# Kernel tuning notes

Measured on AMD Instinct MI355X. Metric: run time of the kernel, lower is better.

Reference implementation:

```python
import jax, jax.numpy as jnp
import numpy as np

K = 9
SIGMA = 4.0
RADIUS = 16  # round(4*sigma)
IMAGE_SHAPE = (256, 256)


def _gaussian_kernel_1d():
    i = jnp.arange(2 * RADIUS + 1, dtype=jnp.float32) - RADIUS
    g = jnp.exp(-(i ** 2) / (2.0 * SIGMA ** 2))
    return g / jnp.sum(g)


def _gaussian_blur(x):
    # x: [b, H, W, 1]; separable Gaussian blur, reflect-101 borders (cv2 default)
    g = _gaussian_kernel_1d()
    xp = jnp.pad(x, ((0, 0), (RADIUS, RADIUS), (RADIUS, RADIUS), (0, 0)), mode='reflect')
    dn = ('NHWC', 'HWIO', 'NHWC')
    kv = g.reshape(2 * RADIUS + 1, 1, 1, 1)  # vertical pass
    kh = g.reshape(1, 2 * RADIUS + 1, 1, 1)  # horizontal pass
    y = jax.lax.conv_general_dilated(xp, kv, (1, 1), 'VALID', dimension_numbers=dn)
    y = jax.lax.conv_general_dilated(y, kh, (1, 1), 'VALID', dimension_numbers=dn)
    return y


def setup_inputs() -> dict:
    key = jax.random.key(0)
    k1, k2 = jax.random.split(key)
    inputs = jax.random.normal(k1, (8, 32, 32, 512), dtype=jnp.float32)
    feature_vector = jax.random.normal(k2, (16384, 512), dtype=jnp.float32)
    return {"inputs": inputs, "feature_vector": feature_vector}


def reference(inputs, feature_vector):
    b, h, w, c = inputs.shape
    feat = inputs.reshape(b * h * w, c)
    # pairwise euclidean distances: [b*h*w, N]
    d2 = (jnp.sum(feat ** 2, axis=-1, keepdims=True)
          + jnp.sum(feature_vector ** 2, axis=-1)[None, :]
          - 2.0 * feat @ feature_vector.T)
    dist = jnp.sqrt(jnp.maximum(d2, 0.0))
    # k smallest distances, ascending (equivalent to tf.sort(...)[..., :k])
    neg_topk, _ = jax.lax.top_k(-dist, K)
    score = -neg_topk  # [b*h*w, K], ascending
    mask = score[:, 0].reshape(b, h, w, 1)
    score = score.reshape(b, h * w, K)
    # patch with maximal nearest-neighbor distance
    idx = jnp.argmax(score[..., 0], axis=-1)  # [b]
    conf = jnp.take_along_axis(score, idx[:, None, None], axis=1)[:, 0, :]  # [b, K]
    exp_conf = jnp.exp(conf)
    weight = 1.0 - jnp.max(exp_conf, axis=-1) / jnp.sum(exp_conf, axis=-1)
    score_out = (jnp.max(score[..., 0], axis=-1) * weight)[:, None]  # [b, 1]
    mask = jax.image.resize(mask, (b, *IMAGE_SHAPE, 1), method='bilinear', antialias=False)
    mask = _gaussian_blur(mask)
    return score_out, mask
```

## Files before the change

### kernel.cpp

```cpp
#include <hip/hip_runtime.h>

typedef __attribute__((ext_vector_type(8))) short bf16x8;
typedef __attribute__((ext_vector_type(4))) float f32x4;

static constexpr int M = 8192;
static constexpr int N = 16384;
static constexpr int K = 512;
static constexpr int BM = 256;
static constexpr int BN = 256;
static constexpr int BK = 64;
static constexpr int KCHUNKS = K / BK;
static constexpr int RBLK = M / BM;
static constexpr int CBLK = N / BN;
static constexpr int BMs = 128;
static constexpr int BKs = 64;
static constexpr int NGROUPS_S = 8;
static constexpr int GROUP_N_S = N / NGROUPS_S;
static constexpr int NTILES_S = GROUP_N_S / 128;
static constexpr float F_INF = 3.0e38f;

__device__ __forceinline__ unsigned short f2bf(float f) {
    unsigned int u = __float_as_uint(f);
    return (unsigned short)((u + 0x7fffu + ((u >> 16) & 1u)) >> 16);
}

__device__ __forceinline__ void gl_lds16(const unsigned short* g, unsigned short* l) {
    __builtin_amdgcn_global_load_lds(
        (const __attribute__((address_space(1))) unsigned int*)g,
        (__attribute__((address_space(3))) unsigned int*)l, 16, 0, 0);
}

__global__ void k_prep(const float* __restrict__ Q, const float* __restrict__ F,
                       unsigned short* __restrict__ Qb, unsigned short* __restrict__ Fb,
                       float* __restrict__ qn, float* __restrict__ fn) {
    int wid = blockIdx.x * 4 + (threadIdx.x >> 6);
    int lane = threadIdx.x & 63;
    bool isQ = wid < M;
    const float* src = isQ ? (Q + (size_t)wid * K) : (F + (size_t)(wid - M) * K);
    unsigned short* dst = isQ ? (Qb + (size_t)wid * K) : (Fb + (size_t)(wid - M) * K);
    const float4* p = reinterpret_cast<const float4*>(src) + lane * 2;
    float4 a = p[0], b = p[1];
    float s = a.x*a.x + a.y*a.y + a.z*a.z + a.w*a.w
            + b.x*b.x + b.y*b.y + b.z*b.z + b.w*b.w;
    bf16x8 v;
    v[0]=(short)f2bf(a.x); v[1]=(short)f2bf(a.y); v[2]=(short)f2bf(a.z); v[3]=(short)f2bf(a.w);
    v[4]=(short)f2bf(b.x); v[5]=(short)f2bf(b.y); v[6]=(short)f2bf(b.z); v[7]=(short)f2bf(b.w);
    *reinterpret_cast<bf16x8*>(dst + lane * 8) = v;
    #pragma unroll
    for (int d = 1; d < 64; d <<= 1) s += __shfl_xor(s, d);
    if (lane == 0) { if (isQ) qn[wid] = s; else fn[wid - M] = s; }
}

__global__ void k_norms(const float* __restrict__ Q, const float* __restrict__ F,
                        float* __restrict__ qn, float* __restrict__ fn) {
    int wid = blockIdx.x * 4 + (threadIdx.x >> 6);
    int lane = threadIdx.x & 63;
    const float* src = (wid < M) ? (Q + (size_t)wid * K) : (F + (size_t)(wid - M) * K);
    const float4* p = reinterpret_cast<const float4*>(src) + lane * 2;
    float4 a = p[0], b = p[1];
    float s = a.x*a.x + a.y*a.y + a.z*a.z + a.w*a.w
            + b.x*b.x + b.y*b.y + b.z*b.z + b.w*b.w;
    #pragma unroll
    for (int d = 1; d < 64; d <<= 1) s += __shfl_xor(s, d);
    if (lane == 0) { if (wid < M) qn[wid] = s; else fn[wid - M] = s; }
}

__global__ __launch_bounds__(512, 2)
void k_mingemm3(const unsigned short* __restrict__ Qb, const unsigned short* __restrict__ Fb,
                const float* __restrict__ qn, const float* __restrict__ fn,
                float* __restrict__ pv, unsigned int* __restrict__ pi) {
    __shared__ unsigned short As[2][BM * BK];
    __shared__ unsigned short Bs[2][BN * BK];
    __shared__ float redv[BM][4];
    __shared__ unsigned int redi[BM][4];

    const int tid = threadIdx.x;
    const int lane = tid & 63;
    const int wave = tid >> 6;
    const int wr = wave >> 2;
    const int wc = wave & 3;
    const int l15 = lane & 15, l4 = lane >> 4;

    const int wg = blockIdx.x;
    const int x = wg & 7, q = wg >> 3;
    const int c_blk = x * 8 + (q & 7);
    const int r_blk = q >> 3;
    const int row0 = r_blk * BM;
    const int col0 = c_blk * BN;

    const int r_l = lane >> 3, p8 = lane & 7;
    const int g8 = p8 ^ r_l;
    const unsigned short* gA[4];
    const unsigned short* gB[4];
    #pragma unroll
    for (int i = 0; i < 4; ++i) {
        int row = wave * 32 + i * 8 + r_l;
        gA[i] = Qb + (size_t)(row0 + row) * K + g8 * 8;
        gB[i] = Fb + (size_t)(col0 + row) * K + g8 * 8;
    }

    auto stage = [&](int kc, int buf) {
        #pragma unroll
        for (int i = 0; i < 4; ++i) gl_lds16(gA[i] + kc * BK, &As[buf][(wave*32 + i*8) * BK]);
        #pragma unroll
        for (int i = 0; i < 4; ++i) gl_lds16(gB[i] + kc * BK, &Bs[buf][(wave*32 + i*8) * BK]);
    };

    f32x4 acc[8][4];
    #pragma unroll
    for (int a = 0; a < 8; ++a)
        #pragma unroll
        for (int b = 0; b < 4; ++b) acc[a][b] = f32x4{0.f, 0.f, 0.f, 0.f};

    stage(0, 0);
    stage(1, 1);
    asm volatile("s_waitcnt vmcnt(8)" ::: "memory");
    __builtin_amdgcn_sched_barrier(0);
    __builtin_amdgcn_s_barrier();

    for (int kc = 0; kc < KCHUNKS; ++kc) {
        const int p = kc & 1;
        bf16x8 af[4][2], bfv[4][2];
        #pragma unroll
        for (int ks = 0; ks < 2; ++ks) {
            const int gidx = ks * 4 + l4;
            #pragma unroll
            for (int fi = 0; fi < 4; ++fi) {
                int r = wr*128 + fi*16 + l15;
                int pg = gidx ^ (r & 7);
                af[fi][ks] = *reinterpret_cast<const bf16x8*>(&As[p][r*BK + pg*8]);
            }
            #pragma unroll
            for (int fj = 0; fj < 4; ++fj) {
                int r = wc*64 + fj*16 + l15;
                int pg = gidx ^ (r & 7);
                bfv[fj][ks] = *reinterpret_cast<const bf16x8*>(&Bs[p][r*BK + pg*8]);
            }
        }
        __builtin_amdgcn_s_setprio(1);
        #pragma unroll
        for (int ks = 0; ks < 2; ++ks)
            #pragma unroll
            for (int fi = 0; fi < 4; ++fi)
                #pragma unroll
                for (int fj = 0; fj < 4; ++fj)
                    acc[fi][fj] = __builtin_amdgcn_mfma_f32_16x16x32_bf16(
                        af[fi][ks], bfv[fj][ks], acc[fi][fj], 0, 0, 0);
        __builtin_amdgcn_s_setprio(0);
        bf16x8 ah[4][2];
        #pragma unroll
        for (int ks = 0; ks < 2; ++ks) {
            const int gidx = ks * 4 + l4;
            #pragma unroll
            for (int fi = 0; fi < 4; ++fi) {
                int r = wr*128 + 64 + fi*16 + l15;
                int pg = gidx ^ (r & 7);
                ah[fi][ks] = *reinterpret_cast<const bf16x8*>(&As[p][r*BK + pg*8]);
            }
        }
        asm volatile("s_waitcnt lgkmcnt(0)" ::: "memory");
        __builtin_amdgcn_sched_barrier(0);
        __builtin_amdgcn_s_barrier();
        if (kc + 2 < KCHUNKS) {
            stage(kc + 2, p);
            asm volatile("s_waitcnt vmcnt(8)" ::: "memory");
        } else {
            asm volatile("s_waitcnt vmcnt(0)" ::: "memory");
        }
        __builtin_amdgcn_sched_barrier(0);
        __builtin_amdgcn_s_barrier();
        __builtin_amdgcn_s_setprio(1);
        #pragma unroll
        for (int ks = 0; ks < 2; ++ks)
            #pragma unroll
            for (int fi = 0; fi < 4; ++fi)
                #pragma unroll
                for (int fj = 0; fj < 4; ++fj)
                    acc[4+fi][fj] = __builtin_amdgcn_mfma_f32_16x16x32_bf16(
                        ah[fi][ks], bfv[fj][ks], acc[4+fi][fj], 0, 0, 0);
        __builtin_amdgcn_s_setprio(0);
    }

    float fnv[4];
    #pragma unroll
    for (int fj = 0; fj < 4; ++fj) fnv[fj] = fn[col0 + wc*64 + fj*16 + l15];
    #pragma unroll
    for (int fi = 0; fi < 8; ++fi) {
        #pragma unroll
        for (int j = 0; j < 4; ++j) {
            int rloc = wr*128 + fi*16 + l4*4 + j;
            float qv = qn[row0 + rloc];
            float v = F_INF; unsigned int ix = 0;
            #pragma unroll
            for (int fj = 0; fj < 4; ++fj) {
                float d2 = qv + fnv[fj] - 2.0f * acc[fi][fj][j];
                if (d2 < v) { v = d2; ix = (unsigned int)(col0 + wc*64 + fj*16 + l15); }
            }
            #pragma unroll
            for (int d = 1; d < 16; d <<= 1) {
                float ov = __shfl_xor(v, d);
                unsigned int oi = (unsigned int)__shfl_xor((int)ix, d);
                if (ov < v) { v = ov; ix = oi; }
            }
            if (l15 == 0) { redv[rloc][wc] = v; redi[rloc][wc] = ix; }
        }
    }
    __syncthreads();
    if (tid < BM) {
        float v = redv[tid][0]; unsigned int ix = redi[tid][0];
        #pragma unroll
        for (int w2 = 1; w2 < 4; ++w2) {
            float ov = redv[tid][w2];
            if (ov < v) { v = ov; ix = redi[tid][w2]; }
        }
        pv[(size_t)(row0 + tid) * CBLK + c_blk] = v;
        pi[(size_t)(row0 + tid) * CBLK + c_blk] = ix;
    }
}

__global__ __launch_bounds__(256, 2)
void k_mingemm_cast(const float* __restrict__ Q, const float* __restrict__ F,
                    const float* __restrict__ qn, const float* __restrict__ fn,
                    float* __restrict__ pv, unsigned int* __restrict__ pi) {
    __shared__ unsigned short As[BMs * BKs];
    __shared__ unsigned short Bs[BMs * BKs];
    __shared__ float qn_t[BMs];
    __shared__ float fn_t[BMs];

    const int tid = threadIdx.x;
    const int lane = tid & 63;
    const int wave = tid >> 6;
    const int wr = wave >> 1, wc = wave & 1;
    const int l15 = lane & 15, l4 = lane >> 4;

    const int row0 = blockIdx.x * BMs;
    const int gbase = blockIdx.y * GROUP_N_S;

    const int srow = tid >> 3;
    const int p8 = tid & 7;
    const int g8 = p8 ^ (srow & 7);
    const float* pA[4];
    const float* pB[4];
    int dstOff[4];
    #pragma unroll
    for (int i = 0; i < 4; ++i) {
        int r = i * 32 + srow;
        pA[i] = Q + (size_t)(row0 + r) * K + g8 * 8;
        pB[i] = F + (size_t)(gbase + r) * K + g8 * 8;
        dstOff[i] = r * BKs + p8 * 8;
    }

    float mval[4][4];
    unsigned int midx[4][4];
    float qnv[4][4];
    #pragma unroll
    for (int a = 0; a < 4; ++a)
        #pragma unroll
        for (int b = 0; b < 4; ++b) { mval[a][b] = F_INF; midx[a][b] = 0; qnv[a][b] = 0.f; }

    for (int nt = 0; nt < NTILES_S; ++nt) {
        f32x4 acc[4][4];
        #pragma unroll
        for (int a = 0; a < 4; ++a)
            #pragma unroll
            for (int b = 0; b < 4; ++b) acc[a][b] = f32x4{0.f, 0.f, 0.f, 0.f};

        for (int kc = 0; kc < KCHUNKS; ++kc) {
            __syncthreads();
            #pragma unroll
            for (int i = 0; i < 4; ++i) {
                const float4* sa = reinterpret_cast<const float4*>(pA[i] + kc * BKs);
                float4 xa = sa[0], ya = sa[1];
                const float4* sb = reinterpret_cast<const float4*>(pB[i] + nt * (128 * K) + kc * BKs);
                float4 xb = sb[0], yb = sb[1];
                bf16x8 va, vb;
                va[0]=(short)f2bf(xa.x); va[1]=(short)f2bf(xa.y); va[2]=(short)f2bf(xa.z); va[3]=(short)f2bf(xa.w);
                va[4]=(short)f2bf(ya.x); va[5]=(short)f2bf(ya.y); va[6]=(short)f2bf(ya.z); va[7]=(short)f2bf(ya.w);
                vb[0]=(short)f2bf(xb.x); vb[1]=(short)f2bf(xb.y); vb[2]=(short)f2bf(xb.z); vb[3]=(short)f2bf(xb.w);
                vb[4]=(short)f2bf(yb.x); vb[5]=(short)f2bf(yb.y); vb[6]=(short)f2bf(yb.z); vb[7]=(short)f2bf(yb.w);
                *reinterpret_cast<bf16x8*>(&As[dstOff[i]]) = va;
                *reinterpret_cast<bf16x8*>(&Bs[dstOff[i]]) = vb;
            }
            if (kc == 0) {
                if (nt == 0 && tid < BMs) qn_t[tid] = qn[row0 + tid];
                if (tid < 128) fn_t[tid] = fn[gbase + nt * 128 + tid];
            }
            __syncthreads();
            if (nt == 0 && kc == 0) {
                #pragma unroll
                for (int fi = 0; fi < 4; ++fi)
                    #pragma unroll
                    for (int j = 0; j < 4; ++j)
                        qnv[fi][j] = qn_t[wr*64 + fi*16 + l4*4 + j];
            }
            #pragma unroll
            for (int ks = 0; ks < 2; ++ks) {
                const int gidx = ks * 4 + l4;
                bf16x8 af[4], bfv[4];
                #pragma unroll
                for (int fi = 0; fi < 4; ++fi) {
                    int r = wr*64 + fi*16 + l15;
                    int pg = gidx ^ (r & 7);
                    af[fi] = *reinterpret_cast<const bf16x8*>(&As[r*BKs + pg*8]);
                }
                #pragma unroll
                for (int fj = 0; fj < 4; ++fj) {
                    int r = wc*64 + fj*16 + l15;
                    int pg = gidx ^ (r & 7);
                    bfv[fj] = *reinterpret_cast<const bf16x8*>(&Bs[r*BKs + pg*8]);
                }
                #pragma unroll
                for (int fi = 0; fi < 4; ++fi)
                    #pragma unroll
                    for (int fj = 0; fj < 4; ++fj)
                        acc[fi][fj] = __builtin_amdgcn_mfma_f32_16x16x32_bf16(
                            af[fi], bfv[fj], acc[fi][fj], 0, 0, 0);
            }
        }
        const int colb = gbase + nt * 128 + wc * 64;
        float fnv[4];
        #pragma unroll
        for (int fj = 0; fj < 4; ++fj) fnv[fj] = fn_t[wc*64 + fj*16 + l15];
        #pragma unroll
        for (int fi = 0; fi < 4; ++fi) {
            #pragma unroll
            for (int j = 0; j < 4; ++j) {
                float qv = qnv[fi][j];
                #pragma unroll
                for (int fj = 0; fj < 4; ++fj) {
                    float d2 = qv + fnv[fj] - 2.0f * acc[fi][fj][j];
                    if (d2 < mval[fi][j]) {
                        mval[fi][j] = d2;
                        midx[fi][j] = (unsigned int)(colb + fj*16 + l15);
                    }
                }
            }
        }
    }
    #pragma unroll
    for (int fi = 0; fi < 4; ++fi) {
        #pragma unroll
        for (int j = 0; j < 4; ++j) {
            float v = mval[fi][j];
            unsigned int ix = midx[fi][j];
            #pragma unroll
            for (int d = 1; d < 16; d <<= 1) {
                float ov = __shfl_xor(v, d);
                unsigned int oi = (unsigned int)__shfl_xor((int)ix, d);
                if (ov < v) { v = ov; ix = oi; }
            }
            if (l15 == 0) {
                int rg = row0 + wr*64 + fi*16 + l4*4 + j;
                int pidx = rg * 16 + blockIdx.y * 2 + wc;
                pv[pidx] = v;
                pi[pidx] = ix;
            }
        }
    }
}

__global__ void k_refine(const float* __restrict__ Q, const float* __restrict__ F,
                         const float* __restrict__ pv, const unsigned int* __restrict__ pi,
                         float* __restrict__ minD, int PS) {
    int row = blockIdx.x * 4 + (threadIdx.x >> 6);
    int lane = threadIdx.x & 63;
    float v = F_INF; unsigned int ix = 0;
    if (lane < PS) { v = pv[(size_t)row*PS + lane]; ix = pi[(size_t)row*PS + lane]; }
    #pragma unroll
    for (int d = 1; d < 64; d <<= 1) {
        float ov = __shfl_xor(v, d);
        unsigned int oi = (unsigned int)__shfl_xor((int)ix, d);
        if (ov < v) { v = ov; ix = oi; }
    }
    const float4* q = reinterpret_cast<const float4*>(Q + (size_t)row * K) + lane*2;
    const float4* f = reinterpret_cast<const float4*>(F + (size_t)ix * K) + lane*2;
    float4 a0 = q[0], a1 = q[1], b0 = f[0], b1 = f[1];
    float s = 0.f, dx;
    dx = a0.x-b0.x; s += dx*dx;  dx = a0.y-b0.y; s += dx*dx;
    dx = a0.z-b0.z; s += dx*dx;  dx = a0.w-b0.w; s += dx*dx;
    dx = a1.x-b1.x; s += dx*dx;  dx = a1.y-b1.y; s += dx*dx;
    dx = a1.z-b1.z; s += dx*dx;  dx = a1.w-b1.w; s += dx*dx;
    #pragma unroll
    for (int d = 1; d < 64; d <<= 1) s += __shfl_xor(s, d);
    if (lane == 0) minD[row] = sqrtf(s);
}

__global__ void k_argmax(const float* __restrict__ minD, unsigned int* __restrict__ sel) {
    __shared__ float sv[256];
    __shared__ int si[256];
    int b = blockIdx.x, tid = threadIdx.x;
    float bv = -F_INF; int bi = 0;
    for (int p = tid; p < 1024; p += 256) {
        float v = minD[b*1024 + p];
        if (v > bv) { bv = v; bi = p; }
    }
    sv[tid] = bv; si[tid] = bi;
    __syncthreads();
    for (int s = 128; s > 0; s >>= 1) {
        if (tid < s) {
            if (sv[tid+s] > sv[tid] || (sv[tid+s] == sv[tid] && si[tid+s] < si[tid])) {
                sv[tid] = sv[tid+s]; si[tid] = si[tid+s];
            }
        }
        __syncthreads();
    }
    if (tid == 0) sel[b] = (unsigned int)(b*1024 + si[0]);
}

__global__ void k_dist8(const float* __restrict__ Q, const float* __restrict__ F,
                        const unsigned int* __restrict__ sel, float* __restrict__ d2all) {
    __shared__ float qs[8][512];
    int tid = threadIdx.x;
    int lane = tid & 63, wave = tid >> 6;
    for (int i = tid; i < 8*512; i += 256) {
        int b = i >> 9;
        qs[b][i & 511] = Q[(size_t)sel[b] * K + (i & 511)];
    }
    __syncthreads();
    int base = blockIdx.x * 128 + wave * 32;
    for (int r = 0; r < 32; ++r) {
        int row = base + r;
        const float4* fp = reinterpret_cast<const float4*>(F + (size_t)row * K) + lane*2;
        float4 f0 = fp[0], f1 = fp[1];
        float fv[8] = {f0.x,f0.y,f0.z,f0.w,f1.x,f1.y,f1.z,f1.w};
        float accb[8];
        #pragma unroll
        for (int b = 0; b < 8; ++b) {
            float s = 0.f;
            #pragma unroll
            for (int e = 0; e < 8; ++e) {
                float d = fv[e] - qs[b][lane*8 + e];
                s += d * d;
            }
            accb[b] = s;
        }
        #pragma unroll
        for (int d = 1; d < 64; d <<= 1)
            #pragma unroll
            for (int b = 0; b < 8; ++b) accb[b] += __shfl_xor(accb[b], d);
        if (lane == 0) {
            #pragma unroll
            for (int b = 0; b < 8; ++b) d2all[b * N + row] = accb[b];
        }
    }
}

__global__ void k_sel9(const float* __restrict__ d2all, float* __restrict__ out) {
    __shared__ float sv[256 * 10];
    int b = blockIdx.x, tid = threadIdx.x;
    float v[9];
    #pragma unroll
    for (int i = 0; i < 9; ++i) v[i] = F_INF;
    for (int i = tid; i < N; i += 256) {
        float x = d2all[b * N + i];
        #pragma unroll
        for (int s = 0; s < 9; ++s) {
            float lo = fminf(v[s], x), hi = fmaxf(v[s], x);
            v[s] = lo; x = hi;
        }
    }
    #pragma unroll
    for (int i = 0; i < 9; ++i) sv[tid*10 + i] = v[i];
    sv[tid*10 + 9] = F_INF;
    __syncthreads();
    for (int s = 128; s > 0; s >>= 1) {
        if (tid < s) {
            int ia = 1, ib = 1;
            float av = sv[tid*10], bv = sv[(tid+s)*10];
            float c[9];
            #pragma unroll
            for (int k = 0; k < 9; ++k) {
                bool ta = av <= bv;
                c[k] = ta ? av : bv;
                float na = sv[tid*10 + ia], nb = sv[(tid+s)*10 + ib];
                if (ta) { av = na; ++ia; } else { bv = nb; ++ib; }
            }
            #pragma unroll
            for (int k = 0; k < 9; ++k) sv[tid*10 + k] = c[k];
        }
        __syncthreads();
    }
    if (tid == 0) {
        float c[9];
        #pragma unroll
        for (int i = 0; i < 9; ++i) c[i] = sqrtf(fmaxf(sv[i], 0.f));
        float S = 0.f;
        #pragma unroll
        for (int i = 0; i < 9; ++i) S += expf(c[i] - c[8]);
        out[b] = c[0] * (1.f - 1.f / S);
    }
}

__global__ void k_top9(const float* __restrict__ Q, const float* __restrict__ F,
                       const unsigned int* __restrict__ sel, float* __restrict__ part9) {
    __shared__ float qs[512];
    __shared__ float dist[2048];
    __shared__ float rv[256];
    __shared__ int ri[256];
    int b = blockIdx.x >> 3, g = blockIdx.x & 7;
    int tid = threadIdx.x;
    unsigned int srow = sel[b];
    if (tid < 128)
        reinterpret_cast<float4*>(qs)[tid] =
            reinterpret_cast<const float4*>(Q + (size_t)srow * K)[tid];
    __syncthreads();
    #pragma unroll
    for (int e = 0; e < 8; ++e) {
        int fl = tid + 256*e;
        const float* fp = F + (size_t)(g*2048 + fl) * K;
        float s = 0.f;
        for (int k = 0; k < 512; k += 4) {
            float4 fv4 = *reinterpret_cast<const float4*>(fp + k);
            float d0 = qs[k]   - fv4.x;
            float d1 = qs[k+1] - fv4.y;
            float d2 = qs[k+2] - fv4.z;
            float d3 = qs[k+3] - fv4.w;
            s += d0*d0 + d1*d1 + d2*d2 + d3*d3;
        }
        dist[fl] = s;
    }
    __syncthreads();
    for (int it = 0; it < 9; ++it) {
        float lv = F_INF; int li = 0;
        #pragma unroll
        for (int e = 0; e < 8; ++e) {
            int idx = tid + 256*e;
            float v = dist[idx];
            if (v < lv) { lv = v; li = idx; }
        }
        rv[tid] = lv; ri[tid] = li;
        __syncthreads();
        for (int s = 128; s > 0; s >>= 1) {
            if (tid < s && rv[tid+s] < rv[tid]) { rv[tid] = rv[tid+s]; ri[tid] = ri[tid+s]; }
            __syncthreads();
        }
        if (tid == 0) {
            part9[(b*8+g)*9 + it] = rv[0];
            dist[ri[0]] = F_INF;
        }
        __syncthreads();
    }
}

__global__ void k_final(const float* __restrict__ part9, float* __restrict__ out) {
    int b = threadIdx.x;
    if (b >= 8) return;
    float arr[9];
    #pragma unroll
    for (int i = 0; i < 9; ++i) arr[i] = F_INF;
    for (int g = 0; g < 8; ++g)
        for (int i = 0; i < 9; ++i) {
            float v = part9[(b*8+g)*9 + i];
            #pragma unroll
            for (int s = 0; s < 9; ++s) {
                float lo = fminf(arr[s], v), hi = fmaxf(arr[s], v);
                arr[s] = lo; v = hi;
            }
        }
    float c[9];
    #pragma unroll
    for (int i = 0; i < 9; ++i) c[i] = sqrtf(fmaxf(arr[i], 0.f));
    float c8 = c[8], S = 0.f;
    #pragma unroll
    for (int i = 0; i < 9; ++i) S += expf(c[i] - c8);
    float w = 1.f - 1.f / S;
    out[b] = c[0] * w;
}

__global__ void k_wmat(float* __restrict__ W) {
    int idx = blockIdx.x * 256 + threadIdx.x;
    int o = idx >> 5, j = idx & 31;
    float gsum = 0.f;
    #pragma unroll
    for (int u = 0; u < 33; ++u) { float d = (float)(u - 16); gsum += expf(-d*d * (1.f/32.f)); }
    float acc = 0.f;
    for (int u = 0; u < 33; ++u) {
        float d = (float)(u - 16);
        float gu = expf(-d*d * (1.f/32.f));
        int y = o + u - 16;
        y = y < 0 ? -y : (y > 255 ? 510 - y : y);
        float xin = ((float)y + 0.5f) * 0.125f - 0.5f;
        float j0f = floorf(xin);
        int j0 = (int)j0f;
        float wfr = xin - j0f;
        float r;
        if (j0 < 0) r = (j == 0) ? 1.f : 0.f;
        else if (j0 >= 31) r = (j == 31) ? 1.f : 0.f;
        else r = (j == j0) ? (1.f - wfr) : ((j == j0 + 1) ? wfr : 0.f);
        acc += gu * r;
    }
    W[idx] = acc / gsum;
}

__global__ void k_mask(const float* __restrict__ minD, const float* __restrict__ W,
                       float* __restrict__ outm) {
    __shared__ float Ms[1024];
    __shared__ float Ws[8192];
    __shared__ float Ts[8192];
    int b = blockIdx.x, tid = threadIdx.x;
    for (int i = tid; i < 1024; i += 256) Ms[i] = minD[b*1024 + i];
    for (int i = tid; i < 8192; i += 256) Ws[i] = W[i];
    __syncthreads();
    {
        int o = tid;
        float wrow[32];
        #pragma unroll
        for (int i = 0; i < 32; ++i) wrow[i] = Ws[o*32 + i];
        for (int j = 0; j < 32; ++j) {
            float s = 0.f;
            #pragma unroll
            for (int i = 0; i < 32; ++i) s += wrow[i] * Ms[i*32 + j];
            Ts[o*32 + j] = s;
        }
    }
    __syncthreads();
    {
        int p = tid;
        float wp[32];
        #pragma unroll
        for (int j = 0; j < 32; ++j) wp[j] = Ws[p*32 + j];
        float* dst = outm + (size_t)b * 65536;
        for (int o = 0; o < 256; ++o) {
            float s = 0.f;
            #pragma unroll
            for (int j = 0; j < 32; ++j) s += Ts[o*32 + j] * wp[j];
            dst[o*256 + p] = s;
        }
    }
}

extern "C" void kernel_launch(void* const* d_in, const int* in_sizes, int n_in,
                              void* d_out, int out_size, void* d_ws, size_t ws_size,
                              hipStream_t stream) {
    const float* Q = (const float*)d_in[0];
    const float* F = (const float*)d_in[1];
    float* out = (float*)d_out;

    const size_t smallFloats = (size_t)8192*64*2 + 8192 + 8 + 576 + (size_t)8*N + 8192 + 16384 + 8192;
    const size_t REQ = smallFloats*4 + (size_t)M*K*2 + (size_t)N*K*2;
    const bool fast = ws_size >= REQ;
    const int PS = fast ? 64 : 16;

    float* ws = (float*)d_ws;
    float* pv = ws;
    unsigned int* pi = (unsigned int*)(pv + 8192*64);
    float* minD = (float*)(pi + 8192*64);
    unsigned int* sel = (unsigned int*)(minD + 8192);
    float* part9 = (float*)(sel + 8);
    float* d2all = part9 + 576;
    float* qn = d2all + (size_t)8*N;
    float* fn = qn + 8192;
    float* W  = fn + 16384;
    unsigned short* Qb = (unsigned short*)(W + 8192);
    unsigned short* Fb = Qb + (size_t)M*K;

    k_wmat <<<dim3(32), 256, 0, stream>>>(W);
    if (fast) {
        k_prep <<<dim3((M + N) / 4), 256, 0, stream>>>(Q, F, Qb, Fb, qn, fn);
        k_mingemm3<<<dim3(RBLK * CBLK), 512, 0, stream>>>(Qb, Fb, qn, fn, pv, pi);
        k_refine<<<dim3(M / 4), 256, 0, stream>>>(Q, F, pv, pi, minD, PS);
        k_argmax<<<dim3(8), 256, 0, stream>>>(minD, sel);
        k_dist8<<<dim3(N / 128), 256, 0, stream>>>(Q, F, sel, d2all);
        k_sel9 <<<dim3(8), 256, 0, stream>>>(d2all, out);
    } else {
        k_norms<<<dim3((M + N) / 4), 256, 0, stream>>>(Q, F, qn, fn);
        k_mingemm_cast<<<dim3(M / BMs, NGROUPS_S), 256, 0, stream>>>(Q, F, qn, fn, pv, pi);
        k_refine<<<dim3(M / 4), 256, 0, stream>>>(Q, F, pv, pi, minD, PS);
        k_argmax<<<dim3(8), 256, 0, stream>>>(minD, sel);
        k_top9 <<<dim3(64), 256, 0, stream>>>(Q, F, sel, part9);
        k_final<<<dim3(1), 64, 0, stream>>>(part9, out);
    }
    k_mask <<<dim3(8), 256, 0, stream>>>(minD, W, out + 8);
}
```

Before: 346.7 us.

## Shrink min-GEMM tiles to 128x128x32 with simpler double-buffered pipeline

Replaces the 256x256 tile, 512-thread min-distance GEMM with a 128x128 tile, BK=32, 256-thread kernel that prefetches the next K slice while computing the current one and issues one barrier per step. The partial-min buffers grow to 128 column blocks per row, and the refine kernel now loops over more than 64 partials. This raises occupancy and parallelism but lowers per-tile data reuse, increases global and LDS traffic, and doubles the partial reduction work.

Result: slower. 367.0 us (+5.9%).

```diff
diff --git a/kernel.cpp b/kernel.cpp
--- a/kernel.cpp
+++ b/kernel.cpp
@@ -6,14 +6,15 @@
 static constexpr int M = 8192;
 static constexpr int N = 16384;
 static constexpr int K = 512;
-static constexpr int BM = 256;
-static constexpr int BN = 256;
-static constexpr int BK = 64;
-static constexpr int KCHUNKS = K / BK;
+static constexpr int BM = 128;
+static constexpr int BN = 128;
+static constexpr int BK = 32;
+static constexpr int KSTEPS = K / BK;
 static constexpr int RBLK = M / BM;
 static constexpr int CBLK = N / BN;
 static constexpr int BMs = 128;
 static constexpr int BKs = 64;
+static constexpr int KCHUNKS_S = K / BKs;
 static constexpr int NGROUPS_S = 8;
 static constexpr int GROUP_N_S = N / NGROUPS_S;
 static constexpr int NTILES_S = GROUP_N_S / 128;
@@ -65,130 +66,93 @@
     if (lane == 0) { if (wid < M) qn[wid] = s; else fn[wid - M] = s; }
 }
 
-__global__ __launch_bounds__(512, 2)
-void k_mingemm3(const unsigned short* __restrict__ Qb, const unsigned short* __restrict__ Fb,
+__global__ __launch_bounds__(256, 4)
+void k_mingemm4(const unsigned short* __restrict__ Qb, const unsigned short* __restrict__ Fb,
                 const float* __restrict__ qn, const float* __restrict__ fn,
                 float* __restrict__ pv, unsigned int* __restrict__ pi) {
     __shared__ unsigned short As[2][BM * BK];
     __shared__ unsigned short Bs[2][BN * BK];
-    __shared__ float redv[BM][4];
-    __shared__ unsigned int redi[BM][4];
+    __shared__ float redv[BM][2];
+    __shared__ unsigned int redi[BM][2];
 
     const int tid = threadIdx.x;
     const int lane = tid & 63;
     const int wave = tid >> 6;
-    const int wr = wave >> 2;
-    const int wc = wave & 3;
+    const int wr = wave >> 1, wc = wave & 1;
     const int l15 = lane & 15, l4 = lane >> 4;
 
     const int wg = blockIdx.x;
     const int x = wg & 7, q = wg >> 3;
-    const int c_blk = x * 8 + (q & 7);
-    const int r_blk = q >> 3;
+    const int c_blk = x * 16 + (q & 15);
+    const int r_blk = q >> 4;
     const int row0 = r_blk * BM;
     const int col0 = c_blk * BN;
 
-    const int r_l = lane >> 3, p8 = lane & 7;
-    const int g8 = p8 ^ r_l;
-    const unsigned short* gA[4];
-    const unsigned short* gB[4];
-    #pragma unroll
-    for (int i = 0; i < 4; ++i) {
-        int row = wave * 32 + i * 8 + r_l;
-        gA[i] = Qb + (size_t)(row0 + row) * K + g8 * 8;
-        gB[i] = Fb + (size_t)(col0 + row) * K + g8 * 8;
+    const int row_l = lane >> 2, p4 = lane & 3;
+    const int g4 = p4 ^ (row_l & 3);
+    const unsigned short* gA[2];
+    const unsigned short* gB[2];
+    #pragma unroll
+    for (int i = 0; i < 2; ++i) {
+        int row = wave * 32 + i * 16 + row_l;
+        gA[i] = Qb + (size_t)(row0 + row) * K + g4 * 8;
+        gB[i] = Fb + (size_t)(col0 + row) * K + g4 * 8;
     }
 
     auto stage = [&](int kc, int buf) {
         #pragma unroll
-        for (int i = 0; i < 4; ++i) gl_lds16(gA[i] + kc * BK, &As[buf][(wave*32 + i*8) * BK]);
-        #pragma unroll
-        for (int i = 0; i < 4; ++i) gl_lds16(gB[i] + kc * BK, &Bs[buf][(wave*32 + i*8) * BK]);
+        for (int i = 0; i < 2; ++i) gl_lds16(gA[i] + kc * BK, &As[buf][(wave*32 + i*16) * BK]);
+        #pragma unroll
+        for (int i = 0; i < 2; ++i) gl_lds16(gB[i] + kc * BK, &Bs[buf][(wave*32 + i*16) * BK]);
     };
 
-    f32x4 acc[8][4];
-    #pragma unroll
-    for (int a = 0; a < 8; ++a)
+    f32x4 acc[4][4];
+    #pragma unroll
+    for (int a = 0; a < 4; ++a)
         #pragma unroll
         for (int b = 0; b < 4; ++b) acc[a][b] = f32x4{0.f, 0.f, 0.f, 0.f};
 
     stage(0, 0);
-    stage(1, 1);
-    asm volatile("s_waitcnt vmcnt(8)" ::: "memory");
-    __builtin_amdgcn_sched_barrier(0);
-    __builtin_amdgcn_s_barrier();
-
-    for (int kc = 0; kc < KCHUNKS; ++kc) {
-        const int p = kc & 1;
-        bf16x8 af[4][2], bfv[4][2];
-        #pragma unroll
-        for (int ks = 0; ks < 2; ++ks) {
-            const int gidx = ks * 4 + l4;
-            #pragma unroll
-            for (int fi = 0; fi < 4; ++fi) {
-                int r = wr*128 + fi*16 + l15;
-                int pg = gidx ^ (r & 7);
-                af[fi][ks] = *reinterpret_cast<const bf16x8*>(&As[p][r*BK + pg*8]);
-            }
-            #pragma unroll
-            for (int fj = 0; fj < 4; ++fj) {
-                int r = wc*64 + fj*16 + l15;
-                int pg = gidx ^ (r & 7);
-                bfv[fj][ks] = *reinterpret_cast<const bf16x8*>(&Bs[p][r*BK + pg*8]);
-            }
+    __syncthreads();
+
+    int cur = 0;
+    for (int kc = 0; kc < KSTEPS; ++kc) {
+        if (kc + 1 < KSTEPS) stage(kc + 1, cur ^ 1);
+        __builtin_amdgcn_sched_barrier(0);
+        const int gidx = l4;
+        bf16x8 af[4], bfv[4];
+        #pragma unroll
+        for (int fi = 0; fi < 4; ++fi) {
+            int r = wr*64 + fi*16 + l15;
+            int pg = gidx ^ (r & 3);
+            af[fi] = *reinterpret_cast<const bf16x8*>(&As[cur][r*BK + pg*8]);
+        }
+        #pragma unroll
+        for (int fj = 0; fj < 4; ++fj) {
+            int r = wc*64 + fj*16 + l15;
+            int pg = gidx ^ (r & 3);
+            bfv[fj] = *reinterpret_cast<const bf16x8*>(&Bs[cur][r*BK + pg*8]);
         }
         __builtin_amdgcn_s_setprio(1);
         #pragma unroll
-        for (int ks = 0; ks < 2; ++ks)
-            #pragma unroll
-            for (int fi = 0; fi < 4; ++fi)
-                #pragma unroll
-                for (int fj = 0; fj < 4; ++fj)
-                    acc[fi][fj] = __builtin_amdgcn_mfma_f32_16x16x32_bf16(
-                        af[fi][ks], bfv[fj][ks], acc[fi][fj], 0, 0, 0);
+        for (int fi = 0; fi < 4; ++fi)
+            #pragma unroll
+            for (int fj = 0; fj < 4; ++fj)
+                acc[fi][fj] = __builtin_amdgcn_mfma_f32_16x16x32_bf16(
+                    af[fi], bfv[fj], acc[fi][fj], 0, 0, 0);
         __builtin_amdgcn_s_setprio(0);
-        bf16x8 ah[4][2];
-        #pragma unroll
-        for (int ks = 0; ks < 2; ++ks) {
-            const int gidx = ks * 4 + l4;
-            #pragma unroll
-            for (int fi = 0; fi < 4; ++fi) {
-                int r = wr*128 + 64 + fi*16 + l15;
-                int pg = gidx ^ (r & 7);
-                ah[fi][ks] = *reinterpret_cast<const bf16x8*>(&As[p][r*BK + pg*8]);
-            }
-        }
-        asm volatile("s_waitcnt lgkmcnt(0)" ::: "memory");
-        __builtin_amdgcn_sched_barrier(0);
-        __builtin_amdgcn_s_barrier();
-        if (kc + 2 < KCHUNKS) {
-            stage(kc + 2, p);
-            asm volatile("s_waitcnt vmcnt(8)" ::: "memory");
-        } else {
-            asm volatile("s_waitcnt vmcnt(0)" ::: "memory");
-        }
-        __builtin_amdgcn_sched_barrier(0);
-        __builtin_amdgcn_s_barrier();
-        __builtin_amdgcn_s_setprio(1);
-        #pragma unroll
-        for (int ks = 0; ks < 2; ++ks)
-            #pragma unroll
-            for (int fi = 0; fi < 4; ++fi)
-                #pragma unroll
-                for (int fj = 0; fj < 4; ++fj)
-                    acc[4+fi][fj] = __builtin_amdgcn_mfma_f32_16x16x32_bf16(
-                        ah[fi][ks], bfv[fj][ks], acc[4+fi][fj], 0, 0, 0);
-        __builtin_amdgcn_s_setprio(0);
+        __syncthreads();
+        cur ^= 1;
     }
 
     float fnv[4];
     #pragma unroll
     for (int fj = 0; fj < 4; ++fj) fnv[fj] = fn[col0 + wc*64 + fj*16 + l15];
     #pragma unroll
-    for (int fi = 0; fi < 8; ++fi) {
+    for (int fi = 0; fi < 4; ++fi) {
         #pragma unroll
         for (int j = 0; j < 4; ++j) {
-            int rloc = wr*128 + fi*16 + l4*4 + j;
+            int rloc = wr*64 + fi*16 + l4*4 + j;
             float qv = qn[row0 + rloc];
             float v = F_INF; unsigned int ix = 0;
             #pragma unroll
@@ -208,11 +172,7 @@
     __syncthreads();
     if (tid < BM) {
         float v = redv[tid][0]; unsigned int ix = redi[tid][0];
-        #pragma unroll
-        for (int w2 = 1; w2 < 4; ++w2) {
-            float ov = redv[tid][w2];
-            if (ov < v) { v = ov; ix = redi[tid][w2]; }
-        }
+        if (redv[tid][1] < v) { v = redv[tid][1]; ix = redi[tid][1]; }
         pv[(size_t)(row0 + tid) * CBLK + c_blk] = v;
         pi[(size_t)(row0 + tid) * CBLK + c_blk] = ix;
     }
@@ -265,7 +225,7 @@
             #pragma unroll
             for (int b = 0; b < 4; ++b) acc[a][b] = f32x4{0.f, 0.f, 0.f, 0.f};
 
-        for (int kc = 0; kc < KCHUNKS; ++kc) {
+        for (int kc = 0; kc < KCHUNKS_S; ++kc) {
             __syncthreads();
             #pragma unroll
             for (int i = 0; i < 4; ++i) {
@@ -365,7 +325,10 @@
     int row = blockIdx.x * 4 + (threadIdx.x >> 6);
     int lane = threadIdx.x & 63;
     float v = F_INF; unsigned int ix = 0;
-    if (lane < PS) { v = pv[(size_t)row*PS + lane]; ix = pi[(size_t)row*PS + lane]; }
+    for (int t = lane; t < PS; t += 64) {
+        float nv = pv[(size_t)row*PS + t];
+        if (nv < v) { v = nv; ix = pi[(size_t)row*PS + t]; }
+    }
     #pragma unroll
     for (int d = 1; d < 64; d <<= 1) {
         float ov = __shfl_xor(v, d);
@@ -636,15 +599,15 @@
     const float* F = (const float*)d_in[1];
     float* out = (float*)d_out;
 
-    const size_t smallFloats = (size_t)8192*64*2 + 8192 + 8 + 576 + (size_t)8*N + 8192 + 16384 + 8192;
+    const size_t smallFloats = (size_t)8192*CBLK*2 + 8192 + 8 + 576 + (size_t)8*N + 8192 + 16384 + 8192;
     const size_t REQ = smallFloats*4 + (size_t)M*K*2 + (size_t)N*K*2;
     const bool fast = ws_size >= REQ;
-    const int PS = fast ? 64 : 16;
+    const int PS = fast ? CBLK : 16;
 
     float* ws = (float*)d_ws;
     float* pv = ws;
-    unsigned int* pi = (unsigned int*)(pv + 8192*64);
-    float* minD = (float*)(pi + 8192*64);
+    unsigned int* pi = (unsigned int*)(pv + 8192*CBLK);
+    float* minD = (float*)(pi + 8192*CBLK);
     unsigned int* sel = (unsigned int*)(minD + 8192);
     float* part9 = (float*)(sel + 8);
     float* d2all = part9 + 576;
@@ -657,7 +620,7 @@
     k_wmat <<<dim3(32), 256, 0, stream>>>(W);
     if (fast) {
         k_prep <<<dim3((M + N) / 4), 256, 0, stream>>>(Q, F, Qb, Fb, qn, fn);
-        k_mingemm3<<<dim3(RBLK * CBLK), 512, 0, stream>>>(Qb, Fb, qn, fn, pv, pi);
+        k_mingemm4<<<dim3(RBLK * CBLK), 256, 0, stream>>>(Qb, Fb, qn, fn, pv, pi);
         k_refine<<<dim3(M / 4), 256, 0, stream>>>(Q, F, pv, pi, minD, PS);
         k_argmax<<<dim3(8), 256, 0, stream>>>(minD, sel);
         k_dist8<<<dim3(N / 128), 256, 0, stream>>>(Q, F, sel, d2all);
```
